# Performance work log

Hardware: AMD Instinct MI355X
Metric: run time of the kernel (lower is better)

The kernel has to match this reference:

```python
import jax, jax.numpy as jnp
import numpy as np


def _resize_bilinear(x, h, w):
    # matches F.upsample(mode='bilinear', align_corners=False) (half-pixel centers)
    return jax.image.resize(x, (x.shape[0], x.shape[1], h, w), method='bilinear')


def _build_volume_2d(fl, fr, maxdisp):
    # fl, fr: [B,C,H,W] -> cost [B,D,H,W], D=maxdisp (stride=1)
    B, C, H, W = fl.shape
    d = jnp.arange(maxdisp)
    src = jnp.arange(W)[None, :] - d[:, None]          # [D,W]
    valid = (src >= 0).astype(fl.dtype)
    src_c = jnp.clip(src, 0, W - 1)
    fr_sh = fr[:, :, :, src_c] * valid                  # [B,C,H,D,W]; zeros where w<d
    cost = jnp.abs(fl[:, :, :, None, :] - fr_sh).sum(axis=1)  # [B,H,D,W]
    return jnp.transpose(cost, (0, 2, 1, 3))            # [B,D,H,W]


def _warp(fr, disp):
    # fr: [B,C,H,W]; disp: [B,K,H,W] horizontal disparity (sample at x - disp)
    # bilinear along W, zero padding (grid_sample semantics, align_corners=True grid)
    B, C, H, W = fr.shape
    xs = jnp.arange(W, dtype=fr.dtype)[None, None, None, :] - disp   # [B,K,H,W]
    x0 = jnp.floor(xs)
    w1 = xs - x0                                        # frac weight for right neighbor
    x0i = x0.astype(jnp.int32)
    x1i = x0i + 1
    v0 = ((x0i >= 0) & (x0i < W)).astype(fr.dtype)
    v1 = ((x1i >= 0) & (x1i < W)).astype(fr.dtype)
    x0c = jnp.clip(x0i, 0, W - 1)
    x1c = jnp.clip(x1i, 0, W - 1)

    def gather(idx):  # idx [B,K,H,W] -> [B,K,C,H,W]
        idxb = jnp.broadcast_to(idx[:, :, None, :, :], (B, idx.shape[1], C, H, W))
        return jnp.take_along_axis(fr[:, None], idxb, axis=-1)

    g0 = gather(x0c) * v0[:, :, None]
    g1 = gather(x1c) * v1[:, :, None]
    return g0 * (1.0 - w1)[:, :, None] + g1 * w1[:, :, None]   # [B,K,C,H,W]


def _build_volume_2d3(fl, fr, maxdisp, disp):
    # fl, fr: [B,C,H,W]; disp: [B,1,H,W] coarse disparity. K = 2*maxdisp-1 shifts.
    shifts = jnp.arange(-maxdisp + 1, maxdisp, dtype=fl.dtype)       # [K]
    bd = disp - shifts[None, :, None, None]                          # [B,K,H,W]
    warped = _warp(fr, bd)                                           # [B,K,C,H,W]
    return jnp.abs(fl[:, None] - warped).sum(axis=2)                 # [B,K,H,W]


def _regress(cost, start, end):
    # softmax(-cost) over disparity axis, weighted sum with disp values [start,end)
    p = jax.nn.softmax(-cost, axis=1)
    dvals = jnp.arange(start, end, dtype=cost.dtype)[None, :, None, None]
    return jnp.sum(p * dvals, axis=1, keepdims=True)                 # [B,1,H,W]


def setup_inputs() -> dict:
    key = jax.random.key(0)
    k = jax.random.split(key, 4)
    return {
        "feat_l0": jax.random.normal(k[0], (4, 32, 64, 128), dtype=jnp.float32),
        "feat_r0": jax.random.normal(k[1], (4, 32, 64, 128), dtype=jnp.float32),
        "feat_l1": jax.random.normal(k[2], (4, 32, 128, 256), dtype=jnp.float32),
        "feat_r1": jax.random.normal(k[3], (4, 32, 128, 256), dtype=jnp.float32),
        "img_h": 512,
        "img_w": 1024,
        "maxdisp0": 12,
        "maxdisp1": 3,
    }


def reference(feat_l0, feat_r0, feat_l1, feat_r1, img_h, img_w, maxdisp0, maxdisp1):
    H0 = feat_l0.shape[2]
    H1, W1 = feat_l1.shape[2], feat_l1.shape[3]

    cost0 = _build_volume_2d(feat_l0, feat_r0, maxdisp0)             # [B,D0,H0,W0]
    pred_low0 = _regress(cost0, 0, maxdisp0) * (img_h / H0)
    pred0 = _resize_bilinear(pred_low0, img_h, img_w)                # [B,1,img_h,img_w]

    # ---- scale 1: residual cost volume via warp around coarse disparity ----
    wflow = _resize_bilinear(pred0, H1, W1) * (H1 / img_h)           # [B,1,H1,W1]
    cost1 = _build_volume_2d3(feat_l1, feat_r1, maxdisp1, wflow)     # [B,2*D1-1,H1,W1]
    pred_low1 = _regress(cost1, -maxdisp1 + 1, maxdisp1) * (img_h / H1)
    pred1 = _resize_bilinear(pred_low1, img_h, img_w) + pred0

    return (pred0, pred1)
```

## Files before the change

kernel.cpp:

```cpp
#include <hip/hip_runtime.h>

#define NB 4
#define NC 32
#define H0 64
#define W0 128
#define D0 12
#define H1 128
#define W1 256
#define NK 5
#define IMH 512
#define IMW 1024

#define FR0_STRIDE 84
#define FR0_GUARD  16
#define FR1_STRIDE 288
#define FR1_GUARD  28

typedef __attribute__((address_space(3))) uint32_t as3_u32;
typedef const __attribute__((address_space(1))) uint32_t as1_u32;

__global__ __launch_bounds__(512) void k_cost0(const float* __restrict__ fl,
                                               const float* __restrict__ fr,
                                               float* __restrict__ pl0) {
    const int blk = blockIdx.x;
    const int row = blk >> 1;
    const int half = blk & 1;
    const int w0 = half * 64;
    const int b = row >> 6, h = row & (H0 - 1);
    const int tid = threadIdx.x;
    __shared__ float frs[NC][FR0_STRIDE];

    const size_t rowbase = ((size_t)b * NC * H0 + h) * W0;

    const int wloc = tid >> 3, g = tid & 7;

    float flv[4];
#pragma unroll
    for (int j = 0; j < 4; ++j)
        flv[j] = fl[rowbase + (size_t)(g + 8 * j) * (H0 * W0) + w0 + wloc];

#pragma unroll
    for (int i = 0; i < 2; ++i) {
        int idx = i * 512 + tid;
        if (idx < NC * 20) {
            int c = idx / 20, q = idx - c * 20;
            int colg = w0 - 16 + q * 4;
            float4 v = make_float4(0.f, 0.f, 0.f, 0.f);
            if (colg >= 0)
                v = *(const float4*)(fr + rowbase + (size_t)c * (H0 * W0) + colg);
            *(float4*)&frs[c][q * 4] = v;
        }
    }
    __syncthreads();

    float cost[D0];
#pragma unroll
    for (int d = 0; d < D0; ++d) cost[d] = 0.f;
#pragma unroll
    for (int j = 0; j < 4; ++j) {
        int c = g + 8 * j;
        const float* sr = &frs[c][FR0_GUARD + wloc];
#pragma unroll
        for (int d = 0; d < D0; ++d)
            cost[d] += fabsf(flv[j] - sr[-d]);
    }
#pragma unroll
    for (int d = 0; d < D0; ++d) {
        cost[d] += __shfl_xor(cost[d], 1);
        cost[d] += __shfl_xor(cost[d], 2);
        cost[d] += __shfl_xor(cost[d], 4);
    }
    if (g == 0) {
        float m = cost[0];
#pragma unroll
        for (int d = 1; d < D0; ++d) m = fminf(m, cost[d]);
        float s = 0.f, sd = 0.f;
#pragma unroll
        for (int d = 0; d < D0; ++d) {
            float e = expf(m - cost[d]);
            s += e;
            sd += (float)d * e;
        }
        pl0[(size_t)row * W0 + w0 + wloc] = 8.f * (sd / s);
    }
}

__global__ __launch_bounds__(512) void k_cost1(const float* __restrict__ fl,
                                               const float* __restrict__ fr,
                                               const float* __restrict__ pl0,
                                               float* __restrict__ pl1) {
    const int blk = blockIdx.x;
    const int b = blk >> 7, oy = blk & (H1 - 1);
    const int tid = threadIdx.x;
    __shared__ float frs1p[NC][FR1_STRIDE];
    __shared__ float ytmp[W0];
    __shared__ float wfl[W1];

    const size_t rowbase1 = ((size_t)b * NC * H1 + oy) * W1;

    {
        const int wave = tid >> 6, lane = tid & 63;
#pragma unroll
        for (int j = 0; j < 4; ++j) {
            int c = wave * 4 + j;
            const float* src = fr + rowbase1 + (size_t)c * (H1 * W1) + lane * 4;
            as3_u32* dst = (as3_u32*)(&frs1p[c][FR1_GUARD]);
            __builtin_amdgcn_global_load_lds((as1_u32*)src, dst, 16, 0, 0);
        }
    }

    const int w = tid >> 1, hh = tid & 1;
    float flv[16];
#pragma unroll
    for (int j = 0; j < 16; ++j)
        flv[j] = fl[rowbase1 + (size_t)(2 * j + hh) * (H1 * W1) + w];

#pragma unroll
    for (int i = 0; i < 2; ++i) {
        int idx = i * 512 + tid;
        int r = idx >> 5, q = idx & 31;
        int col = (q < FR1_GUARD) ? q : (FR1_GUARD + W1 + (q - FR1_GUARD));
        frs1p[r][col] = 0.f;
    }

    if (tid < W0) {
        const float* p0b = pl0 + (size_t)b * H0 * W0;
        int m = oy >> 1;
        int r0, r1, r2;
        float wy0, wy1, wy2;
        if (oy == 0) {
            r0 = 0; r1 = 0; r2 = 1;
            wy0 = 0.f; wy1 = 27.625f / 28.f; wy2 = 0.375f / 28.f;
        } else if (oy == H1 - 1) {
            r0 = H0 - 2; r1 = H0 - 1; r2 = H0 - 1;
            wy0 = 0.375f / 28.f; wy1 = 27.625f / 28.f; wy2 = 0.f;
        } else {
            r0 = max(m - 1, 0); r1 = m; r2 = min(m + 1, H0 - 1);
            if (oy & 1) { wy0 = 0.375f / 32.f; wy1 = 23.25f / 32.f; wy2 = 8.375f / 32.f; }
            else        { wy0 = 8.375f / 32.f; wy1 = 23.25f / 32.f; wy2 = 0.375f / 32.f; }
        }
        ytmp[tid] = wy0 * p0b[r0 * W0 + tid] + wy1 * p0b[r1 * W0 + tid]
                  + wy2 * p0b[r2 * W0 + tid];
    }
    __syncthreads();

    if (tid < W1) {
        int ox = tid, n = ox >> 1;
        int c0, c1, c2;
        float wx0, wx1, wx2;
        if (ox == 0) {
            c0 = 0; c1 = 0; c2 = 1;
            wx0 = 0.f; wx1 = 27.625f / 28.f; wx2 = 0.375f / 28.f;
        } else if (ox == W1 - 1) {
            c0 = W0 - 2; c1 = W0 - 1; c2 = W0 - 1;
            wx0 = 0.375f / 28.f; wx1 = 27.625f / 28.f; wx2 = 0.f;
        } else {
            c0 = max(n - 1, 0); c1 = n; c2 = min(n + 1, W0 - 1);
            if (ox & 1) { wx0 = 0.375f / 32.f; wx1 = 23.25f / 32.f; wx2 = 8.375f / 32.f; }
            else        { wx0 = 8.375f / 32.f; wx1 = 23.25f / 32.f; wx2 = 0.375f / 32.f; }
        }
        wfl[ox] = 0.25f * (wx0 * ytmp[c0] + wx1 * ytmp[c1] + wx2 * ytmp[c2]);
    }
    __syncthreads();

    {
        float disp = wfl[w];
        float xs = (float)w - disp;
        float xbf = floorf(xs);
        float f = xs - xbf;
        int xb = (int)xbf;
        const float* sr = &frs1p[0][FR1_GUARD + xb - 2];

        float cost[NK];
#pragma unroll
        for (int k = 0; k < NK; ++k) cost[k] = 0.f;
#pragma unroll
        for (int j = 0; j < 16; ++j) {
            int c = 2 * j + hh;
            const float* row = sr + c * FR1_STRIDE;
            float g0 = row[0], g1 = row[1], g2 = row[2];
            float g3 = row[3], g4 = row[4], g5 = row[5];
            float flvj = flv[j];
            cost[0] += fabsf(flvj - (g0 + f * (g1 - g0)));
            cost[1] += fabsf(flvj - (g1 + f * (g2 - g1)));
            cost[2] += fabsf(flvj - (g2 + f * (g3 - g2)));
            cost[3] += fabsf(flvj - (g3 + f * (g4 - g3)));
            cost[4] += fabsf(flvj - (g5 * f + g4 * (1.f - f)));
        }
#pragma unroll
        for (int k = 0; k < NK; ++k) cost[k] += __shfl_xor(cost[k], 1);
        if (hh == 0) {
            float m = cost[0];
#pragma unroll
            for (int k = 1; k < NK; ++k) m = fminf(m, cost[k]);
            float s = 0.f, sd = 0.f;
#pragma unroll
            for (int k = 0; k < NK; ++k) {
                float e = expf(m - cost[k]);
                s += e;
                sd += (float)(k - 2) * e;
            }
            pl1[(size_t)blk * W1 + w] = 4.f * (sd / s);
        }
    }
}

__global__ __launch_bounds__(256) void k_final(const float* __restrict__ pl0,
                                               const float* __restrict__ pl1,
                                               float* __restrict__ out) {
    const int blk = blockIdx.x;
    const int b = blk >> 9, y = blk & (IMH - 1);
    const int tid = threadIdx.x;
    __shared__ float a0[W0];
    __shared__ float a1[W1];

    const float* p0b = pl0 + (size_t)b * H0 * W0;
    const float* p1b = pl1 + (size_t)b * H1 * W1;

    float sy0 = (y + 0.5f) * 0.125f - 0.5f;
    float y0f = floorf(sy0);
    float fy0 = sy0 - y0f;
    int r0 = (int)y0f;
    int r0c = min(max(r0, 0), H0 - 1), r1c = min(max(r0 + 1, 0), H0 - 1);

    float sy1 = (y + 0.5f) * 0.25f - 0.5f;
    float y1f = floorf(sy1);
    float fy1 = sy1 - y1f;
    int s0 = (int)y1f;
    int s0c = min(max(s0, 0), H1 - 1), s1c = min(max(s0 + 1, 0), H1 - 1);

    if (tid < W0) {
        float u = p0b[r0c * W0 + tid], v = p0b[r1c * W0 + tid];
        a0[tid] = u + fy0 * (v - u);
    }
    {
        float u = p1b[s0c * W1 + tid], v = p1b[s1c * W1 + tid];
        a1[tid] = u + fy1 * (v - u);
    }
    __syncthreads();

    float v0[4], v1[4];
#pragma unroll
    for (int i = 0; i < 4; ++i) {
        int x = tid * 4 + i;
        float sx0 = (x + 0.5f) * 0.125f - 0.5f;
        float x0f = floorf(sx0);
        float fx0 = sx0 - x0f;
        int c0 = (int)x0f;
        int c0c = min(max(c0, 0), W0 - 1), c1c = min(max(c0 + 1, 0), W0 - 1);
        float p0 = a0[c0c] + fx0 * (a0[c1c] - a0[c0c]);

        float sx1 = (x + 0.5f) * 0.25f - 0.5f;
        float x1f = floorf(sx1);
        float fx1 = sx1 - x1f;
        int d0 = (int)x1f;
        int d0c = min(max(d0, 0), W1 - 1), d1c = min(max(d0 + 1, 0), W1 - 1);
        float p1 = a1[d0c] + fx1 * (a1[d1c] - a1[d0c]);

        v0[i] = p0;
        v1[i] = p1 + p0;
    }
    const size_t NPXQ = (size_t)NB * IMH * IMW / 4;
    size_t t = (size_t)blk * 256 + tid;
    ((float4*)out)[t] = make_float4(v0[0], v0[1], v0[2], v0[3]);
    ((float4*)out)[NPXQ + t] = make_float4(v1[0], v1[1], v1[2], v1[3]);
}

extern "C" void kernel_launch(void* const* d_in, const int* in_sizes, int n_in,
                              void* d_out, int out_size, void* d_ws, size_t ws_size,
                              hipStream_t stream) {
    const float* fl0 = (const float*)d_in[0];
    const float* fr0 = (const float*)d_in[1];
    const float* fl1 = (const float*)d_in[2];
    const float* fr1 = (const float*)d_in[3];
    float* out = (float*)d_out;

    float* ws = (float*)d_ws;
    float* pl0 = ws;
    float* pl1 = ws + 32768;

    k_cost0<<<NB * H0 * 2, 512, 0, stream>>>(fl0, fr0, pl0);
    k_cost1<<<NB * H1, 512, 0, stream>>>(fl1, fr1, pl0, pl1);
    k_final<<<NB * IMH, 256, 0, stream>>>(pl0, pl1, out);
}
```

Before: 26.27 us.

## Fuse scale-0 and scale-1 cost kernels, recomputing neighbor coarse rows per block

Merges the two cost-volume kernels into one launch. Each block handles one coarse row and recomputes the scale-0 regression for three neighboring rows in shared memory, so it can build the vertical upsample of the coarse disparity locally without a global round trip or kernel boundary. Each block then processes two fine rows of the scale-1 residual cost volume. This removes a launch and the dependency on global pl0 between stages, at the cost of triple redundant scale-0 compute, much larger shared memory per block, and only 256 blocks. It also adds a min-blocks hint to k_final's launch bounds.

```diff
diff --git a/kernel.cpp b/kernel.cpp
--- a/kernel.cpp
+++ b/kernel.cpp
@@ -11,141 +11,128 @@
 #define IMH 512
 #define IMW 1024
 
-#define FR0_STRIDE 84
-#define FR0_GUARD  16
-#define FR1_STRIDE 288
-#define FR1_GUARD  28
+#define S0L 144
+#define G0L 16
+#define S1L 288
+#define G1L 28
 
 typedef __attribute__((address_space(3))) uint32_t as3_u32;
 typedef const __attribute__((address_space(1))) uint32_t as1_u32;
 
-__global__ __launch_bounds__(512) void k_cost0(const float* __restrict__ fl,
-                                               const float* __restrict__ fr,
-                                               float* __restrict__ pl0) {
-    const int blk = blockIdx.x;
-    const int row = blk >> 1;
-    const int half = blk & 1;
-    const int w0 = half * 64;
-    const int b = row >> 6, h = row & (H0 - 1);
+__global__ __launch_bounds__(512) void k_main(
+        const float* __restrict__ fl0, const float* __restrict__ fr0,
+        const float* __restrict__ fl1, const float* __restrict__ fr1,
+        float* __restrict__ pl0, float* __restrict__ pl1) {
+    const int bk = blockIdx.x;
+    const int b = bk >> 6, m = bk & 63;
     const int tid = threadIdx.x;
-    __shared__ float frs[NC][FR0_STRIDE];
-
-    const size_t rowbase = ((size_t)b * NC * H0 + h) * W0;
-
-    const int wloc = tid >> 3, g = tid & 7;
-
-    float flv[4];
-#pragma unroll
-    for (int j = 0; j < 4; ++j)
-        flv[j] = fl[rowbase + (size_t)(g + 8 * j) * (H0 * W0) + w0 + wloc];
-
-#pragma unroll
-    for (int i = 0; i < 2; ++i) {
+    const int wave = tid >> 6, lane = tid & 63;
+
+    __shared__ float frs1[2][NC][S1L];
+    __shared__ float frs0[3][NC][S0L];
+    __shared__ float p0l[3][W0];
+    __shared__ float ytmp[2][W0];
+    __shared__ float wfl[2][W1];
+
+#pragma unroll
+    for (int j = 0; j < 8; ++j) {
+        int idx = wave * 8 + j;
+        int it = idx >> 5, c = idx & 31;
+        const float* src = fr1 + ((size_t)(b * NC + c) * H1 + (2 * m + it)) * W1
+                         + lane * 4;
+        as3_u32* dst = (as3_u32*)&frs1[it][c][G1L];
+        __builtin_amdgcn_global_load_lds((as1_u32*)src, dst, 16, 0, 0);
+    }
+    {
+        int it = tid >> 8, c = (tid >> 3) & 31, u = tid & 7;
+        int col = (u < 7) ? u * 4 : (G1L + W1);
+        *(float4*)&frs1[it][c][col] = make_float4(0.f, 0.f, 0.f, 0.f);
+    }
+
+#pragma unroll
+    for (int i = 0; i < 6; ++i) {
         int idx = i * 512 + tid;
-        if (idx < NC * 20) {
-            int c = idx / 20, q = idx - c * 20;
-            int colg = w0 - 16 + q * 4;
-            float4 v = make_float4(0.f, 0.f, 0.f, 0.f);
-            if (colg >= 0)
-                v = *(const float4*)(fr + rowbase + (size_t)c * (H0 * W0) + colg);
-            *(float4*)&frs[c][q * 4] = v;
-        }
-    }
-    __syncthreads();
-
-    float cost[D0];
-#pragma unroll
-    for (int d = 0; d < D0; ++d) cost[d] = 0.f;
-#pragma unroll
-    for (int j = 0; j < 4; ++j) {
-        int c = g + 8 * j;
-        const float* sr = &frs[c][FR0_GUARD + wloc];
-#pragma unroll
-        for (int d = 0; d < D0; ++d)
-            cost[d] += fabsf(flv[j] - sr[-d]);
-    }
-#pragma unroll
-    for (int d = 0; d < D0; ++d) {
-        cost[d] += __shfl_xor(cost[d], 1);
-        cost[d] += __shfl_xor(cost[d], 2);
-        cost[d] += __shfl_xor(cost[d], 4);
-    }
-    if (g == 0) {
-        float m = cost[0];
-#pragma unroll
-        for (int d = 1; d < D0; ++d) m = fminf(m, cost[d]);
-        float s = 0.f, sd = 0.f;
+        int rr = idx >> 10, rem = idx & 1023, c = rem >> 5, q = rem & 31;
+        int row = min(max(m - 1 + rr, 0), H0 - 1);
+        float4 v = *(const float4*)(fr0 + ((size_t)(b * NC + c) * H0 + row) * W0
+                                    + q * 4);
+        *(float4*)&frs0[rr][c][G0L + q * 4] = v;
+    }
+    if (tid < 384) {
+        int rr = tid >> 7, c = (tid >> 2) & 31, u = tid & 3;
+        *(float4*)&frs0[rr][c][u * 4] = make_float4(0.f, 0.f, 0.f, 0.f);
+    }
+
+    const int w0g = tid >> 2, g = tid & 3;
+    float flv0[3][8];
+#pragma unroll
+    for (int rr = 0; rr < 3; ++rr) {
+        int row = min(max(m - 1 + rr, 0), H0 - 1);
+#pragma unroll
+        for (int j = 0; j < 8; ++j)
+            flv0[rr][j] = fl0[((size_t)(b * NC + 4 * j + g) * H0 + row) * W0 + w0g];
+    }
+    const int w1 = tid >> 1, hh = tid & 1;
+    float flv1[2][16];
+#pragma unroll
+    for (int it = 0; it < 2; ++it)
+#pragma unroll
+        for (int j = 0; j < 16; ++j)
+            flv1[it][j] = fl1[((size_t)(b * NC + 2 * j + hh) * H1 + 2 * m + it) * W1
+                              + w1];
+    __syncthreads();
+
+#pragma unroll
+    for (int rr = 0; rr < 3; ++rr) {
+        float cost[D0];
+#pragma unroll
+        for (int d = 0; d < D0; ++d) cost[d] = 0.f;
+#pragma unroll
+        for (int j = 0; j < 8; ++j) {
+            const float* sr = &frs0[rr][4 * j + g][G0L + w0g];
+            float fv = flv0[rr][j];
+#pragma unroll
+            for (int d = 0; d < D0; ++d)
+                cost[d] += fabsf(fv - sr[-d]);
+        }
 #pragma unroll
         for (int d = 0; d < D0; ++d) {
-            float e = expf(m - cost[d]);
-            s += e;
-            sd += (float)d * e;
-        }
-        pl0[(size_t)row * W0 + w0 + wloc] = 8.f * (sd / s);
-    }
-}
-
-__global__ __launch_bounds__(512) void k_cost1(const float* __restrict__ fl,
-                                               const float* __restrict__ fr,
-                                               const float* __restrict__ pl0,
-                                               float* __restrict__ pl1) {
-    const int blk = blockIdx.x;
-    const int b = blk >> 7, oy = blk & (H1 - 1);
-    const int tid = threadIdx.x;
-    __shared__ float frs1p[NC][FR1_STRIDE];
-    __shared__ float ytmp[W0];
-    __shared__ float wfl[W1];
-
-    const size_t rowbase1 = ((size_t)b * NC * H1 + oy) * W1;
-
+            cost[d] += __shfl_xor(cost[d], 1);
+            cost[d] += __shfl_xor(cost[d], 2);
+        }
+        if (g == 0) {
+            float mn = cost[0];
+#pragma unroll
+            for (int d = 1; d < D0; ++d) mn = fminf(mn, cost[d]);
+            float s = 0.f, sd = 0.f;
+#pragma unroll
+            for (int d = 0; d < D0; ++d) {
+                float e = expf(mn - cost[d]);
+                s += e;
+                sd += (float)d * e;
+            }
+            float val = 8.f * (sd / s);
+            p0l[rr][w0g] = val;
+            if (rr == 1)
+                pl0[((size_t)b * H0 + m) * W0 + w0g] = val;
+        }
+    }
+    __syncthreads();
+
+    if (tid < 256) {
+        int it = tid >> 7, col = tid & 127;
+        int oy = 2 * m + it;
+        float wy0, wy1, wy2;
+        if (oy == 0)            { wy0 = 0.f;            wy1 = 27.625f / 28.f; wy2 = 0.375f / 28.f; }
+        else if (oy == H1 - 1)  { wy0 = 0.375f / 28.f;  wy1 = 27.625f / 28.f; wy2 = 0.f; }
+        else if (oy & 1)        { wy0 = 0.375f / 32.f;  wy1 = 23.25f / 32.f;  wy2 = 8.375f / 32.f; }
+        else                    { wy0 = 8.375f / 32.f;  wy1 = 23.25f / 32.f;  wy2 = 0.375f / 32.f; }
+        ytmp[it][col] = wy0 * p0l[0][col] + wy1 * p0l[1][col] + wy2 * p0l[2][col];
+    }
+    __syncthreads();
     {
-        const int wave = tid >> 6, lane = tid & 63;
-#pragma unroll
-        for (int j = 0; j < 4; ++j) {
-            int c = wave * 4 + j;
-            const float* src = fr + rowbase1 + (size_t)c * (H1 * W1) + lane * 4;
-            as3_u32* dst = (as3_u32*)(&frs1p[c][FR1_GUARD]);
-            __builtin_amdgcn_global_load_lds((as1_u32*)src, dst, 16, 0, 0);
-        }
-    }
-
-    const int w = tid >> 1, hh = tid & 1;
-    float flv[16];
-#pragma unroll
-    for (int j = 0; j < 16; ++j)
-        flv[j] = fl[rowbase1 + (size_t)(2 * j + hh) * (H1 * W1) + w];
-
-#pragma unroll
-    for (int i = 0; i < 2; ++i) {
-        int idx = i * 512 + tid;
-        int r = idx >> 5, q = idx & 31;
-        int col = (q < FR1_GUARD) ? q : (FR1_GUARD + W1 + (q - FR1_GUARD));
-        frs1p[r][col] = 0.f;
-    }
-
-    if (tid < W0) {
-        const float* p0b = pl0 + (size_t)b * H0 * W0;
-        int m = oy >> 1;
-        int r0, r1, r2;
-        float wy0, wy1, wy2;
-        if (oy == 0) {
-            r0 = 0; r1 = 0; r2 = 1;
-            wy0 = 0.f; wy1 = 27.625f / 28.f; wy2 = 0.375f / 28.f;
-        } else if (oy == H1 - 1) {
-            r0 = H0 - 2; r1 = H0 - 1; r2 = H0 - 1;
-            wy0 = 0.375f / 28.f; wy1 = 27.625f / 28.f; wy2 = 0.f;
-        } else {
-            r0 = max(m - 1, 0); r1 = m; r2 = min(m + 1, H0 - 1);
-            if (oy & 1) { wy0 = 0.375f / 32.f; wy1 = 23.25f / 32.f; wy2 = 8.375f / 32.f; }
-            else        { wy0 = 8.375f / 32.f; wy1 = 23.25f / 32.f; wy2 = 0.375f / 32.f; }
-        }
-        ytmp[tid] = wy0 * p0b[r0 * W0 + tid] + wy1 * p0b[r1 * W0 + tid]
-                  + wy2 * p0b[r2 * W0 + tid];
-    }
-    __syncthreads();
-
-    if (tid < W1) {
-        int ox = tid, n = ox >> 1;
+        int it = tid >> 8, ox = tid & 255;
+        int n = ox >> 1;
         int c0, c1, c2;
         float wx0, wx1, wx2;
         if (ox == 0) {
@@ -159,55 +146,56 @@
             if (ox & 1) { wx0 = 0.375f / 32.f; wx1 = 23.25f / 32.f; wx2 = 8.375f / 32.f; }
             else        { wx0 = 8.375f / 32.f; wx1 = 23.25f / 32.f; wx2 = 0.375f / 32.f; }
         }
-        wfl[ox] = 0.25f * (wx0 * ytmp[c0] + wx1 * ytmp[c1] + wx2 * ytmp[c2]);
-    }
-    __syncthreads();
-
-    {
-        float disp = wfl[w];
-        float xs = (float)w - disp;
+        wfl[it][ox] = 0.25f * (wx0 * ytmp[it][c0] + wx1 * ytmp[it][c1]
+                             + wx2 * ytmp[it][c2]);
+    }
+    __syncthreads();
+
+#pragma unroll
+    for (int it = 0; it < 2; ++it) {
+        float disp = wfl[it][w1];
+        float xs = (float)w1 - disp;
         float xbf = floorf(xs);
         float f = xs - xbf;
         int xb = (int)xbf;
-        const float* sr = &frs1p[0][FR1_GUARD + xb - 2];
+        const float* sr = &frs1[it][0][G1L + xb - 2];
 
         float cost[NK];
 #pragma unroll
         for (int k = 0; k < NK; ++k) cost[k] = 0.f;
 #pragma unroll
         for (int j = 0; j < 16; ++j) {
-            int c = 2 * j + hh;
-            const float* row = sr + c * FR1_STRIDE;
+            const float* row = sr + (2 * j + hh) * S1L;
             float g0 = row[0], g1 = row[1], g2 = row[2];
             float g3 = row[3], g4 = row[4], g5 = row[5];
-            float flvj = flv[j];
-            cost[0] += fabsf(flvj - (g0 + f * (g1 - g0)));
-            cost[1] += fabsf(flvj - (g1 + f * (g2 - g1)));
-            cost[2] += fabsf(flvj - (g2 + f * (g3 - g2)));
-            cost[3] += fabsf(flvj - (g3 + f * (g4 - g3)));
-            cost[4] += fabsf(flvj - (g5 * f + g4 * (1.f - f)));
+            float fv = flv1[it][j];
+            cost[0] += fabsf(fv - (g0 + f * (g1 - g0)));
+            cost[1] += fabsf(fv - (g1 + f * (g2 - g1)));
+            cost[2] += fabsf(fv - (g2 + f * (g3 - g2)));
+            cost[3] += fabsf(fv - (g3 + f * (g4 - g3)));
+            cost[4] += fabsf(fv - (g5 * f + g4 * (1.f - f)));
         }
 #pragma unroll
         for (int k = 0; k < NK; ++k) cost[k] += __shfl_xor(cost[k], 1);
         if (hh == 0) {
-            float m = cost[0];
-#pragma unroll
-            for (int k = 1; k < NK; ++k) m = fminf(m, cost[k]);
+            float mn = cost[0];
+#pragma unroll
+            for (int k = 1; k < NK; ++k) mn = fminf(mn, cost[k]);
             float s = 0.f, sd = 0.f;
 #pragma unroll
             for (int k = 0; k < NK; ++k) {
-                float e = expf(m - cost[k]);
+                float e = expf(mn - cost[k]);
                 s += e;
                 sd += (float)(k - 2) * e;
             }
-            pl1[(size_t)blk * W1 + w] = 4.f * (sd / s);
+            pl1[((size_t)b * H1 + 2 * m + it) * W1 + w1] = 4.f * (sd / s);
         }
     }
 }
 
-__global__ __launch_bounds__(256) void k_final(const float* __restrict__ pl0,
-                                               const float* __restrict__ pl1,
-                                               float* __restrict__ out) {
+__global__ __launch_bounds__(256, 4) void k_final(const float* __restrict__ pl0,
+                                                  const float* __restrict__ pl1,
+                                                  float* __restrict__ out) {
     const int blk = blockIdx.x;
     const int b = blk >> 9, y = blk & (IMH - 1);
     const int tid = threadIdx.x;
@@ -279,7 +267,6 @@
     float* pl0 = ws;
     float* pl1 = ws + 32768;
 
-    k_cost0<<<NB * H0 * 2, 512, 0, stream>>>(fl0, fr0, pl0);
-    k_cost1<<<NB * H1, 512, 0, stream>>>(fl1, fr1, pl0, pl1);
+    k_main<<<NB * H0, 512, 0, stream>>>(fl0, fr0, fl1, fr1, pl0, pl1);
     k_final<<<NB * IMH, 256, 0, stream>>>(pl0, pl1, out);
 }
```

After: 30.45 us. 1.16x slower.
